# Performance work log

Hardware: AMD Instinct MI355X
Metric: run time of the kernel (lower is better)

The kernel has to match this reference:

```python
import jax, jax.numpy as jnp
import numpy as np

N = 50000
E = 800000
IN_C = 64
OUT_C = 64
K = 2
GATE_C = IN_C + OUT_C
LAMBDA_MAX = 2.0


def _lap_norm(edge_index, edge_weight, n):
    # PyG ChebConv norm: sym Laplacian L = I - D^-1/2 A D^-1/2, scaled 2L/lmax - I.
    # With lambda_max=2 the diagonal term is (2/lmax)*1 - 1 = 0, so only the
    # off-diagonal weights -(2/lmax) * w_norm remain.
    row, col = edge_index[0], edge_index[1]
    deg = jax.ops.segment_sum(edge_weight, row, num_segments=n)
    dinv = jnp.where(deg > 0, jax.lax.rsqrt(jnp.where(deg > 0, deg, 1.0)), 0.0)
    lw = -(2.0 / LAMBDA_MAX) * edge_weight * dinv[row] * dinv[col]
    diag = jnp.full((n,), 2.0 / LAMBDA_MAX - 1.0, edge_weight.dtype)  # zeros for lmax=2
    return row, col, lw, diag


def _cheb_conv(x, row, col, lw, diag, Ws, b):
    # Ws: [K, C_in, C_out]; Tx_0 = x, Tx_1 = L_hat x, Tx_k = 2 L_hat Tx_{k-1} - Tx_{k-2}
    n = x.shape[0]

    def prop(h):  # L_hat @ h  via edge gather/scatter + diagonal
        msg = lw[:, None] * h[col]                      # [E, C]
        return jax.ops.segment_sum(msg, row, num_segments=n) + diag[:, None] * h

    Tx0 = x
    out = Tx0 @ Ws[0]
    Tx1 = prop(x)
    out = out + Tx1 @ Ws[1]
    for k in range(2, K):
        Tx2 = 2.0 * prop(Tx1) - Tx0
        out = out + Tx2 @ Ws[k]
        Tx0, Tx1 = Tx1, Tx2
    return out + b


def setup_inputs() -> dict:
    key = jax.random.key(0)
    ks = jax.random.split(key, 10)
    scale = 1.0 / np.sqrt(GATE_C)
    x = jax.random.normal(ks[0], (N, IN_C), jnp.float32)
    edge_index = jax.random.randint(ks[1], (2, E), 0, N, jnp.int64)
    edge_weight = jax.random.uniform(ks[2], (E,), jnp.float32)
    hidden_state = jax.random.normal(ks[3], (N, OUT_C), jnp.float32)
    Wz = jax.random.normal(ks[4], (K, GATE_C, OUT_C), jnp.float32) * scale
    Wr = jax.random.normal(ks[5], (K, GATE_C, OUT_C), jnp.float32) * scale
    Wh = jax.random.normal(ks[6], (K, GATE_C, OUT_C), jnp.float32) * scale
    bz = jnp.zeros((OUT_C,), jnp.float32)
    br = jnp.zeros((OUT_C,), jnp.float32)
    bh = jnp.zeros((OUT_C,), jnp.float32)
    return {"x": x, "edge_index": edge_index, "edge_weight": edge_weight,
            "hidden_state": hidden_state, "Wz": Wz, "bz": bz,
            "Wr": Wr, "br": br, "Wh": Wh, "bh": bh}


def reference(x, edge_index, edge_weight, hidden_state, Wz, bz, Wr, br, Wh, bh):
    n = x.shape[0]
    row, col, lw, diag = _lap_norm(edge_index, edge_weight, n)
    gate_input = jnp.concatenate([x, hidden_state], axis=-1)          # [N, GATE_C]
    z = jax.nn.sigmoid(_cheb_conv(gate_input, row, col, lw, diag, Wz, bz))
    r = jax.nn.sigmoid(_cheb_conv(gate_input, row, col, lw, diag, Wr, br))
    cand_in = jnp.concatenate([x, r * hidden_state], axis=-1)
    h_tilde = jnp.tanh(_cheb_conv(cand_in, row, col, lw, diag, Wh, bh))
    return (1.0 - z) * hidden_state + z * h_tilde
```

## Files before the change

### kernel.cpp

```cpp
#include <hip/hip_runtime.h>
#include <cstdint>

#define N_NODES 50000
#define N_EDGES 800000
#define C 64
#define SLOTS 64
#define B_N 120
#define NB 417
#define PCAP 2560
#define STG_BLOCKS 126
#define STG_CHUNK 6350

typedef __attribute__((ext_vector_type(8))) short bf16x8;
typedef __attribute__((ext_vector_type(4))) float f32x4;

static constexpr size_t OFF_GCUR = 0;
static constexpr size_t OFF_DINV = 512;
static constexpr size_t OFF_CNT  = 50688;
static constexpr size_t OFF_BZR  = 100864;
static constexpr size_t OFF_BH   = 117248;
static constexpr size_t OFF_CSR  = 125440;
static constexpr size_t OFF_XH   = OFF_CSR + (size_t)N_NODES * 64;
static constexpr size_t OFF_XB   = OFF_XH + (size_t)N_NODES * C;
static constexpr size_t OFF_HB   = OFF_XB + (size_t)N_NODES * C / 2;
static constexpr size_t OFF_PXB  = OFF_HB + (size_t)N_NODES * C / 2;
static constexpr size_t OFF_PHB  = OFF_PXB + (size_t)N_NODES * C / 2;
static constexpr size_t OFF_RHB  = OFF_PHB + (size_t)N_NODES * C / 2;
static constexpr size_t OFF_RHD  = OFF_RHB + (size_t)N_NODES * C / 2;
static constexpr size_t OFF_STG  = OFF_PXB;

__device__ __forceinline__ short f2bf(float f) {
    unsigned u = __float_as_uint(f);
    u += 0x7fffu + ((u >> 16) & 1u);
    return (short)(u >> 16);
}
__device__ __forceinline__ float bf_lo(unsigned v) { return __uint_as_float(v << 16); }
__device__ __forceinline__ float bf_hi(unsigned v) { return __uint_as_float(v & 0xffff0000u); }
__device__ __forceinline__ float bfu(unsigned short v) { return __uint_as_float((unsigned)v << 16); }
__device__ __forceinline__ float fast_sigmoid(float v) { return 1.f / (1.f + __expf(-v)); }
__device__ __forceinline__ float fast_tanh(float v) { return 1.f - 2.f / (__expf(2.f * v) + 1.f); }

__global__ __launch_bounds__(256) void zero_pack_kernel(
        int* __restrict__ gcur,
        const float* __restrict__ Wz, const float* __restrict__ Wr,
        const float* __restrict__ Wh,
        short* __restrict__ Bzr, short* __restrict__ Bh) {
    if (blockIdx.x == 24) {
        gcur[threadIdx.x] = 0;
        gcur[256 + threadIdx.x] = 0;
        return;
    }
    int gid = blockIdx.x * 256 + threadIdx.x;
    if (gid < 4096) {
        int ktct = gid >> 6, lane = gid & 63;
        int kt = ktct >> 3, ct = ktct & 7;
        int colg = ct * 16 + (lane & 15);
        int k0 = kt * 32 + (lane >> 4) * 8;
        const float* W = (colg < 64) ? Wz : Wr;
        int c = colg & 63;
        short v[8];
        #pragma unroll
        for (int j = 0; j < 8; ++j) {
            int k = k0 + j;
            v[j] = f2bf(W[(k >> 7) * (128 * 64) + (k & 127) * 64 + c]);
        }
        *(bf16x8*)(Bzr + (size_t)ktct * 512 + lane * 8) = *(bf16x8*)v;
    } else {
        int idx = gid - 4096;
        int ktct = idx >> 6, lane = idx & 63;
        int kt = ktct >> 2, ct = ktct & 3;
        int colg = ct * 16 + (lane & 15);
        int k0 = kt * 32 + (lane >> 4) * 8;
        short v[8];
        #pragma unroll
        for (int j = 0; j < 8; ++j) {
            int k = k0 + j;
            v[j] = f2bf(Wh[(k >> 7) * (128 * 64) + (k & 127) * 64 + colg]);
        }
        *(bf16x8*)(Bh + (size_t)ktct * 512 + lane * 8) = *(bf16x8*)v;
    }
}

__global__ __launch_bounds__(512) void stage_kernel(
        const int* __restrict__ row, const int* __restrict__ col,
        const float* __restrict__ w,
        int* __restrict__ gcur, uint2* __restrict__ stg) {
    __shared__ int lcnt[NB];
    __shared__ int lbase[NB];
    int tid = threadIdx.x;
    int e0 = blockIdx.x * STG_CHUNK;
    int e1 = min(e0 + STG_CHUNK, N_EDGES);
    for (int i = tid; i < NB; i += 512) lcnt[i] = 0;
    __syncthreads();
    for (int e = e0 + tid; e < e1; e += 512)
        atomicAdd(&lcnt[row[e] / B_N], 1);
    __syncthreads();
    for (int i = tid; i < NB; i += 512) {
        int c = lcnt[i];
        lbase[i] = c ? atomicAdd(&gcur[i], c) : 0;
        lcnt[i] = 0;
    }
    __syncthreads();
    for (int e = e0 + tid; e < e1; e += 512) {
        int r = row[e];
        int b = r / B_N;
        int off = atomicAdd(&lcnt[b], 1);
        int pos = lbase[b] + off;
        unsigned cw = ((unsigned)col[e] << 16) | (unsigned short)f2bf(w[e]);
        if (pos < PCAP)
            stg[(size_t)b * PCAP + pos] = make_uint2((unsigned)(r - b * B_N), cw);
    }
}

__global__ __launch_bounds__(256) void sort_kernel(
        const int* __restrict__ gcur, const uint2* __restrict__ stg,
        const float* __restrict__ x, const float* __restrict__ h,
        unsigned* __restrict__ csr, int* __restrict__ cnt, float* __restrict__ dinv,
        unsigned* __restrict__ xh,
        unsigned short* __restrict__ xb, unsigned short* __restrict__ hb) {
    __shared__ int lcnt[B_N];
    __shared__ int lbase[B_N];
    __shared__ float ldeg[B_N];
    __shared__ float ldv[B_N];
    __shared__ int scanb[128];
    __shared__ unsigned lbuf[PCAP];
    __shared__ unsigned char lnode[PCAP];
    int b = blockIdx.x, tid = threadIdx.x;
    int n0 = b * B_N;
    int m = min(gcur[b], PCAP);
    for (int i = tid; i < B_N; i += 256) { lcnt[i] = 0; ldeg[i] = 0.f; }
    __syncthreads();
    const uint2* s = stg + (size_t)b * PCAP;
    for (int i = tid; i < m; i += 256) {
        uint2 e = s[i];
        atomicAdd(&lcnt[e.x], 1);
        atomicAdd(&ldeg[e.x], bf_lo(e.y));
    }
    __syncthreads();
    if (tid < 128) scanb[tid] = (tid < B_N) ? lcnt[tid] : 0;
    __syncthreads();
    for (int d = 1; d < 128; d <<= 1) {
        int v = 0;
        if (tid < 128 && tid >= d) v = scanb[tid - d];
        __syncthreads();
        if (tid < 128) scanb[tid] += v;
        __syncthreads();
    }
    if (tid < B_N) { lbase[tid] = scanb[tid] - lcnt[tid]; lcnt[tid] = 0; }
    __syncthreads();
    for (int i = tid; i < m; i += 256) {
        uint2 e = s[i];
        int off = atomicAdd(&lcnt[e.x], 1);
        int p = lbase[e.x] + off;
        lbuf[p] = e.y;
        lnode[p] = (unsigned char)e.x;
    }
    __syncthreads();
    for (int i = tid; i < m; i += 256) {
        int nl = lnode[i];
        int pos = i - lbase[nl];
        csr[(size_t)(n0 + nl) * SLOTS + pos] = lbuf[i];
    }
    for (int i = tid; i < B_N * 8; i += 256) {
        int nl = i >> 3;
        int node = n0 + nl;
        if (node >= N_NODES) continue;
        int mm = min(lcnt[nl], SLOTS);
        int pe = (mm + 7) & ~7;
        int idx = mm + (i & 7);
        if (idx < pe) csr[(size_t)node * SLOTS + idx] = 0u;
    }
    if (tid < B_N) {
        int node = n0 + tid;
        if (node < N_NODES) {
            cnt[node] = lcnt[tid];
            float d = ldeg[tid];
            float dv = (d > 0.f) ? rsqrtf(d) : 0.f;
            dinv[node] = dv;
            ldv[tid] = dv;
        } else ldv[tid] = 0.f;
    }
    __syncthreads();
    for (int i = tid; i < B_N * 16; i += 256) {
        int g = n0 * 16 + i;
        if (g >= N_NODES * 16) continue;
        float dv = ldv[i >> 4];
        float4 xv = ((const float4*)x)[g];
        float4 hv = ((const float4*)h)[g];
        uint4 o;
        o.x = ((unsigned)(unsigned short)f2bf(hv.x * dv) << 16) | (unsigned short)f2bf(xv.x * dv);
        o.y = ((unsigned)(unsigned short)f2bf(hv.y * dv) << 16) | (unsigned short)f2bf(xv.y * dv);
        o.z = ((unsigned)(unsigned short)f2bf(hv.z * dv) << 16) | (unsigned short)f2bf(xv.z * dv);
        o.w = ((unsigned)(unsigned short)f2bf(hv.w * dv) << 16) | (unsigned short)f2bf(xv.w * dv);
        ((uint4*)xh)[g] = o;
        ((short4*)xb)[g] = make_short4(f2bf(xv.x), f2bf(xv.y), f2bf(xv.z), f2bf(xv.w));
        ((short4*)hb)[g] = make_short4(f2bf(hv.x), f2bf(hv.y), f2bf(hv.z), f2bf(hv.w));
    }
}

__global__ __launch_bounds__(256) void prop_gemm_zr_kernel(
        const int* __restrict__ cnt, const unsigned* __restrict__ csr,
        const float* __restrict__ dinv, const unsigned* __restrict__ xh,
        const unsigned short* __restrict__ xb, const unsigned short* __restrict__ hb,
        const short* __restrict__ Bzr,
        const float* __restrict__ bz, const float* __restrict__ br,
        unsigned short* __restrict__ Pxb,
        float* __restrict__ z, unsigned short* __restrict__ rhb,
        unsigned short* __restrict__ rhd) {
    __shared__ __align__(16) unsigned short lpx[16][72];
    __shared__ __align__(16) unsigned short lph[16][72];
    int tid = threadIdx.x;
    int wid = tid >> 6, lane = tid & 63;
    int node0 = blockIdx.x * 16;

    #pragma unroll
    for (int i = 0; i < 2; ++i) {
        int nlA = wid * 4 + i * 2;
        int nA = node0 + nlA;
        int2 cc = *(const int2*)(cnt + nA);
        int gqA = (min(cc.x, SLOTS) + 7) >> 3;
        int gqB = (min(cc.y, SLOTS) + 7) >> 3;
        const uint4* sA = (const uint4*)(csr + (size_t)nA * SLOTS);
        const uint4* sB = (const uint4*)(csr + (size_t)(nA + 1) * SLOTS);
        float axA = 0.f, ahA = 0.f, axB = 0.f, ahB = 0.f;
        int gmax = max(gqA, gqB);
        for (int g = 0; g < gmax; ++g) {
            bool doA = g < gqA, doB = g < gqB;
            uint4 a0, a1, b0, b1;
            unsigned va0, va1, va2, va3, va4, va5, va6, va7;
            unsigned vb0, vb1, vb2, vb3, vb4, vb5, vb6, vb7;
            if (doA) { a0 = sA[2 * g]; a1 = sA[2 * g + 1]; }
            if (doB) { b0 = sB[2 * g]; b1 = sB[2 * g + 1]; }
            if (doA) {
                va0 = xh[(a0.x >> 16) * C + lane];
                va1 = xh[(a0.y >> 16) * C + lane];
                va2 = xh[(a0.z >> 16) * C + lane];
                va3 = xh[(a0.w >> 16) * C + lane];
                va4 = xh[(a1.x >> 16) * C + lane];
                va5 = xh[(a1.y >> 16) * C + lane];
                va6 = xh[(a1.z >> 16) * C + lane];
                va7 = xh[(a1.w >> 16) * C + lane];
            }
            if (doB) {
                vb0 = xh[(b0.x >> 16) * C + lane];
                vb1 = xh[(b0.y >> 16) * C + lane];
                vb2 = xh[(b0.z >> 16) * C + lane];
                vb3 = xh[(b0.w >> 16) * C + lane];
                vb4 = xh[(b1.x >> 16) * C + lane];
                vb5 = xh[(b1.y >> 16) * C + lane];
                vb6 = xh[(b1.z >> 16) * C + lane];
                vb7 = xh[(b1.w >> 16) * C + lane];
            }
            if (doA) {
                float w0 = bf_lo(a0.x), w1 = bf_lo(a0.y), w2 = bf_lo(a0.z), w3 = bf_lo(a0.w);
                float w4 = bf_lo(a1.x), w5 = bf_lo(a1.y), w6 = bf_lo(a1.z), w7 = bf_lo(a1.w);
                axA = fmaf(w0, bf_lo(va0), axA);  ahA = fmaf(w0, bf_hi(va0), ahA);
                axA = fmaf(w1, bf_lo(va1), axA);  ahA = fmaf(w1, bf_hi(va1), ahA);
                axA = fmaf(w2, bf_lo(va2), axA);  ahA = fmaf(w2, bf_hi(va2), ahA);
                axA = fmaf(w3, bf_lo(va3), axA);  ahA = fmaf(w3, bf_hi(va3), ahA);
                axA = fmaf(w4, bf_lo(va4), axA);  ahA = fmaf(w4, bf_hi(va4), ahA);
                axA = fmaf(w5, bf_lo(va5), axA);  ahA = fmaf(w5, bf_hi(va5), ahA);
                axA = fmaf(w6, bf_lo(va6), axA);  ahA = fmaf(w6, bf_hi(va6), ahA);
                axA = fmaf(w7, bf_lo(va7), axA);  ahA = fmaf(w7, bf_hi(va7), ahA);
            }
            if (doB) {
                float w0 = bf_lo(b0.x), w1 = bf_lo(b0.y), w2 = bf_lo(b0.z), w3 = bf_lo(b0.w);
                float w4 = bf_lo(b1.x), w5 = bf_lo(b1.y), w6 = bf_lo(b1.z), w7 = bf_lo(b1.w);
                axB = fmaf(w0, bf_lo(vb0), axB);  ahB = fmaf(w0, bf_hi(vb0), ahB);
                axB = fmaf(w1, bf_lo(vb1), axB);  ahB = fmaf(w1, bf_hi(vb1), ahB);
                axB = fmaf(w2, bf_lo(vb2), axB);  ahB = fmaf(w2, bf_hi(vb2), ahB);
                axB = fmaf(w3, bf_lo(vb3), axB);  ahB = fmaf(w3, bf_hi(vb3), ahB);
                axB = fmaf(w4, bf_lo(vb4), axB);  ahB = fmaf(w4, bf_hi(vb4), ahB);
                axB = fmaf(w5, bf_lo(vb5), axB);  ahB = fmaf(w5, bf_hi(vb5), ahB);
                axB = fmaf(w6, bf_lo(vb6), axB);  ahB = fmaf(w6, bf_hi(vb6), ahB);
                axB = fmaf(w7, bf_lo(vb7), axB);  ahB = fmaf(w7, bf_hi(vb7), ahB);
            }
        }
        float2 dv = *(const float2*)(dinv + nA);
        unsigned short pxA = (unsigned short)f2bf(-dv.x * axA);
        unsigned short phA = (unsigned short)f2bf(-dv.x * ahA);
        unsigned short pxB = (unsigned short)f2bf(-dv.y * axB);
        unsigned short phB = (unsigned short)f2bf(-dv.y * ahB);
        lpx[nlA][lane] = pxA;      lph[nlA][lane] = phA;
        lpx[nlA + 1][lane] = pxB;  lph[nlA + 1][lane] = phB;
        Pxb[(size_t)nA * C + lane] = pxA;
        Pxb[(size_t)(nA + 1) * C + lane] = pxB;
    }
    __syncthreads();

    int q = lane >> 4;
    int nl = lane & 15;
    f32x4 acc[2];
    acc[0] = (f32x4){0.f, 0.f, 0.f, 0.f};
    acc[1] = (f32x4){0.f, 0.f, 0.f, 0.f};
    const bf16x8* Bp = (const bf16x8*)Bzr;
    #pragma unroll
    for (int kt = 0; kt < 8; ++kt) {
        bf16x8 a;
        if (kt < 4) {
            const unsigned short* src = (kt < 2) ? xb : hb;
            a = *(const bf16x8*)(src + (size_t)(node0 + nl) * C + (kt & 1) * 32 + q * 8);
        } else {
            const unsigned short* src = (kt < 6) ? &lpx[0][0] : &lph[0][0];
            a = *(const bf16x8*)(src + nl * 72 + (kt & 1) * 32 + q * 8);
        }
        #pragma unroll
        for (int c2 = 0; c2 < 2; ++c2) {
            int ct = wid * 2 + c2;
            bf16x8 bfr = Bp[(kt * 8 + ct) * 64 + lane];
            acc[c2] = __builtin_amdgcn_mfma_f32_16x16x32_bf16(a, bfr, acc[c2], 0, 0, 0);
        }
    }

    if (wid < 2) {
        #pragma unroll
        for (int c2 = 0; c2 < 2; ++c2) {
            int colg = (wid * 2 + c2) * 16 + nl;
            float bias = bz[colg];
            #pragma unroll
            for (int r = 0; r < 4; ++r) {
                int node = node0 + q * 4 + r;
                z[(size_t)node * C + colg] = fast_sigmoid(acc[c2][r] + bias);
            }
        }
    } else {
        float dv[4];
        #pragma unroll
        for (int r = 0; r < 4; ++r) dv[r] = dinv[node0 + q * 4 + r];
        #pragma unroll
        for (int c2 = 0; c2 < 2; ++c2) {
            int oc = (wid * 2 + c2 - 4) * 16 + nl;
            float bias = br[oc];
            #pragma unroll
            for (int r = 0; r < 4; ++r) {
                int node = node0 + q * 4 + r;
                float sg = fast_sigmoid(acc[c2][r] + bias);
                float rhv = sg * bfu(hb[(size_t)node * C + oc]);
                rhb[(size_t)node * C + oc] = (unsigned short)f2bf(rhv);
                rhd[(size_t)node * C + oc] = (unsigned short)f2bf(rhv * dv[r]);
            }
        }
    }
}

__global__ __launch_bounds__(256) void prop_gemm_h_kernel(
        const int* __restrict__ cnt, const unsigned* __restrict__ csr,
        const float* __restrict__ dinv, const unsigned short* __restrict__ rhd,
        const unsigned short* __restrict__ xb, const unsigned short* __restrict__ rhb,
        const unsigned short* __restrict__ Pxb,
        const short* __restrict__ Bh, const float* __restrict__ bh,
        const float* __restrict__ z, const float* __restrict__ h,
        float* __restrict__ out) {
    __shared__ __align__(16) unsigned short lpr[16][72];
    int tid = threadIdx.x;
    int wid = tid >> 6, lane = tid & 63;
    int node0 = blockIdx.x * 16;

    #pragma unroll
    for (int i = 0; i < 2; ++i) {
        int nlA = wid * 4 + i * 2;
        int nA = node0 + nlA;
        int2 cc = *(const int2*)(cnt + nA);
        int gqA = (min(cc.x, SLOTS) + 7) >> 3;
        int gqB = (min(cc.y, SLOTS) + 7) >> 3;
        const uint4* sA = (const uint4*)(csr + (size_t)nA * SLOTS);
        const uint4* sB = (const uint4*)(csr + (size_t)(nA + 1) * SLOTS);
        float accA = 0.f, accB = 0.f;
        int gmax = max(gqA, gqB);
        for (int g = 0; g < gmax; ++g) {
            bool doA = g < gqA, doB = g < gqB;
            uint4 a0, a1, b0, b1;
            unsigned short va0, va1, va2, va3, va4, va5, va6, va7;
            unsigned short vb0, vb1, vb2, vb3, vb4, vb5, vb6, vb7;
            if (doA) { a0 = sA[2 * g]; a1 = sA[2 * g + 1]; }
            if (doB) { b0 = sB[2 * g]; b1 = sB[2 * g + 1]; }
            if (doA) {
                va0 = rhd[(a0.x >> 16) * C + lane];
                va1 = rhd[(a0.y >> 16) * C + lane];
                va2 = rhd[(a0.z >> 16) * C + lane];
                va3 = rhd[(a0.w >> 16) * C + lane];
                va4 = rhd[(a1.x >> 16) * C + lane];
                va5 = rhd[(a1.y >> 16) * C + lane];
                va6 = rhd[(a1.z >> 16) * C + lane];
                va7 = rhd[(a1.w >> 16) * C + lane];
            }
            if (doB) {
                vb0 = rhd[(b0.x >> 16) * C + lane];
                vb1 = rhd[(b0.y >> 16) * C + lane];
                vb2 = rhd[(b0.z >> 16) * C + lane];
                vb3 = rhd[(b0.w >> 16) * C + lane];
                vb4 = rhd[(b1.x >> 16) * C + lane];
                vb5 = rhd[(b1.y >> 16) * C + lane];
                vb6 = rhd[(b1.z >> 16) * C + lane];
                vb7 = rhd[(b1.w >> 16) * C + lane];
            }
            if (doA) {
                accA = fmaf(bf_lo(a0.x), bfu(va0), accA);
                accA = fmaf(bf_lo(a0.y), bfu(va1), accA);
                accA = fmaf(bf_lo(a0.z), bfu(va2), accA);
                accA = fmaf(bf_lo(a0.w), bfu(va3), accA);
                accA = fmaf(bf_lo(a1.x), bfu(va4), accA);
                accA = fmaf(bf_lo(a1.y), bfu(va5), accA);
                accA = fmaf(bf_lo(a1.z), bfu(va6), accA);
                accA = fmaf(bf_lo(a1.w), bfu(va7), accA);
            }
            if (doB) {
                accB = fmaf(bf_lo(b0.x), bfu(vb0), accB);
                accB = fmaf(bf_lo(b0.y), bfu(vb1), accB);
                accB = fmaf(bf_lo(b0.z), bfu(vb2), accB);
                accB = fmaf(bf_lo(b0.w), bfu(vb3), accB);
                accB = fmaf(bf_lo(b1.x), bfu(vb4), accB);
                accB = fmaf(bf_lo(b1.y), bfu(vb5), accB);
                accB = fmaf(bf_lo(b1.z), bfu(vb6), accB);
                accB = fmaf(bf_lo(b1.w), bfu(vb7), accB);
            }
        }
        float2 dv = *(const float2*)(dinv + nA);
        lpr[nlA][lane]     = (unsigned short)f2bf(-dv.x * accA);
        lpr[nlA + 1][lane] = (unsigned short)f2bf(-dv.y * accB);
    }
    __syncthreads();

    int q = lane >> 4;
    int nl = lane & 15;
    f32x4 acc = (f32x4){0.f, 0.f, 0.f, 0.f};
    const bf16x8* Bp = (const bf16x8*)Bh;
    #pragma unroll
    for (int kt = 0; kt < 8; ++kt) {
        bf16x8 a;
        if (kt < 6) {
            const unsigned short* src = (kt < 2) ? xb : (kt < 4) ? rhb : Pxb;
            a = *(const bf16x8*)(src + (size_t)(node0 + nl) * C + (kt & 1) * 32 + q * 8);
        } else {
            a = *(const bf16x8*)(&lpr[0][0] + nl * 72 + (kt & 1) * 32 + q * 8);
        }
        bf16x8 bfr = Bp[(kt * 4 + wid) * 64 + lane];
        acc = __builtin_amdgcn_mfma_f32_16x16x32_bf16(a, bfr, acc, 0, 0, 0);
    }

    int oc = wid * 16 + nl;
    float bias = bh[oc];
    #pragma unroll
    for (int r = 0; r < 4; ++r) {
        int node = node0 + q * 4 + r;
        float ht = fast_tanh(acc[r] + bias);
        float zz = z[(size_t)node * C + oc];
        float hv = h[(size_t)node * C + oc];
        out[(size_t)node * C + oc] = (1.f - zz) * hv + zz * ht;
    }
}

extern "C" void kernel_launch(void* const* d_in, const int* in_sizes, int n_in,
                              void* d_out, int out_size, void* d_ws, size_t ws_size,
                              hipStream_t stream) {
    const float* x    = (const float*)d_in[0];
    const int*   eidx = (const int*)  d_in[1];
    const float* w    = (const float*)d_in[2];
    const float* h    = (const float*)d_in[3];
    const float* Wz   = (const float*)d_in[4];
    const float* bz   = (const float*)d_in[5];
    const float* Wr   = (const float*)d_in[6];
    const float* br   = (const float*)d_in[7];
    const float* Wh   = (const float*)d_in[8];
    const float* bh   = (const float*)d_in[9];
    float* out = (float*)d_out;
    float* ws  = (float*)d_ws;

    const int* row = eidx;
    const int* col = eidx + N_EDGES;

    int*            gcur = (int*)(ws + OFF_GCUR);
    float*          dinv = ws + OFF_DINV;
    int*            cnt  = (int*)(ws + OFF_CNT);
    unsigned*       csr  = (unsigned*)(ws + OFF_CSR);
    short*          Bzr  = (short*)(ws + OFF_BZR);
    short*          Bh   = (short*)(ws + OFF_BH);
    unsigned*       xh   = (unsigned*)(ws + OFF_XH);
    unsigned short* xb   = (unsigned short*)(ws + OFF_XB);
    unsigned short* hb   = (unsigned short*)(ws + OFF_HB);
    unsigned short* Pxb  = (unsigned short*)(ws + OFF_PXB);
    unsigned short* rhb  = (unsigned short*)(ws + OFF_RHB);
    unsigned short* rhd  = (unsigned short*)(ws + OFF_RHD);
    uint2*          stg  = (uint2*)(ws + OFF_STG);
    float*          z    = out;

    zero_pack_kernel<<<25, 256, 0, stream>>>(gcur, Wz, Wr, Wh, Bzr, Bh);

    stage_kernel<<<STG_BLOCKS, 512, 0, stream>>>(row, col, w, gcur, stg);

    sort_kernel<<<NB, 256, 0, stream>>>(gcur, stg, x, h, csr, cnt, dinv, xh, xb, hb);

    prop_gemm_zr_kernel<<<N_NODES / 16, 256, 0, stream>>>(
        cnt, csr, dinv, xh, xb, hb, Bzr, bz, br, Pxb, z, rhb, rhd);

    prop_gemm_h_kernel<<<N_NODES / 16, 256, 0, stream>>>(
        cnt, csr, dinv, rhd, xb, rhb, Pxb, Bh, bh, z, h, out);
}
```

Baseline: 209.9 us.

## Software-pipeline CSR gather loops with double-buffered neighbor loads

```diff
diff --git a/kernel.cpp b/kernel.cpp
--- a/kernel.cpp
+++ b/kernel.cpp
@@ -13,6 +13,8 @@
 
 typedef __attribute__((ext_vector_type(8))) short bf16x8;
 typedef __attribute__((ext_vector_type(4))) float f32x4;
+typedef __attribute__((ext_vector_type(8))) unsigned u32x8;
+typedef __attribute__((ext_vector_type(8))) unsigned short u16x8;
 
 static constexpr size_t OFF_GCUR = 0;
 static constexpr size_t OFF_DINV = 512;
@@ -39,6 +41,41 @@
 __device__ __forceinline__ float bfu(unsigned short v) { return __uint_as_float((unsigned)v << 16); }
 __device__ __forceinline__ float fast_sigmoid(float v) { return 1.f / (1.f + __expf(-v)); }
 __device__ __forceinline__ float fast_tanh(float v) { return 1.f - 2.f / (__expf(2.f * v) + 1.f); }
+
+#define ISS8(buf, q0, q1, TBL) \
+    buf[0] = TBL[(q0.x >> 16) * C + lane]; \
+    buf[1] = TBL[(q0.y >> 16) * C + lane]; \
+    buf[2] = TBL[(q0.z >> 16) * C + lane]; \
+    buf[3] = TBL[(q0.w >> 16) * C + lane]; \
+    buf[4] = TBL[(q1.x >> 16) * C + lane]; \
+    buf[5] = TBL[(q1.y >> 16) * C + lane]; \
+    buf[6] = TBL[(q1.z >> 16) * C + lane]; \
+    buf[7] = TBL[(q1.w >> 16) * C + lane];
+
+#define WEXT(W, q0, q1) \
+    float W##0 = bf_lo(q0.x), W##1 = bf_lo(q0.y), W##2 = bf_lo(q0.z), \
+          W##3 = bf_lo(q0.w), W##4 = bf_lo(q1.x), W##5 = bf_lo(q1.y), \
+          W##6 = bf_lo(q1.z), W##7 = bf_lo(q1.w);
+
+#define FMA2x8(buf, W, ax, ah) \
+    ax = fmaf(W##0, bf_lo(buf[0]), ax); ah = fmaf(W##0, bf_hi(buf[0]), ah); \
+    ax = fmaf(W##1, bf_lo(buf[1]), ax); ah = fmaf(W##1, bf_hi(buf[1]), ah); \
+    ax = fmaf(W##2, bf_lo(buf[2]), ax); ah = fmaf(W##2, bf_hi(buf[2]), ah); \
+    ax = fmaf(W##3, bf_lo(buf[3]), ax); ah = fmaf(W##3, bf_hi(buf[3]), ah); \
+    ax = fmaf(W##4, bf_lo(buf[4]), ax); ah = fmaf(W##4, bf_hi(buf[4]), ah); \
+    ax = fmaf(W##5, bf_lo(buf[5]), ax); ah = fmaf(W##5, bf_hi(buf[5]), ah); \
+    ax = fmaf(W##6, bf_lo(buf[6]), ax); ah = fmaf(W##6, bf_hi(buf[6]), ah); \
+    ax = fmaf(W##7, bf_lo(buf[7]), ax); ah = fmaf(W##7, bf_hi(buf[7]), ah);
+
+#define FMA1x8(buf, W, acc) \
+    acc = fmaf(W##0, bfu(buf[0]), acc); \
+    acc = fmaf(W##1, bfu(buf[1]), acc); \
+    acc = fmaf(W##2, bfu(buf[2]), acc); \
+    acc = fmaf(W##3, bfu(buf[3]), acc); \
+    acc = fmaf(W##4, bfu(buf[4]), acc); \
+    acc = fmaf(W##5, bfu(buf[5]), acc); \
+    acc = fmaf(W##6, bfu(buf[6]), acc); \
+    acc = fmaf(W##7, bfu(buf[7]), acc);
 
 __global__ __launch_bounds__(256) void zero_pack_kernel(
         int* __restrict__ gcur,
@@ -167,6 +204,7 @@
         if (node >= N_NODES) continue;
         int mm = min(lcnt[nl], SLOTS);
         int pe = (mm + 7) & ~7;
+        if (pe == 0) pe = 8;
         int idx = mm + (i & 7);
         if (idx < pe) csr[(size_t)node * SLOTS + idx] = 0u;
     }
@@ -218,62 +256,43 @@
         int nlA = wid * 4 + i * 2;
         int nA = node0 + nlA;
         int2 cc = *(const int2*)(cnt + nA);
-        int gqA = (min(cc.x, SLOTS) + 7) >> 3;
-        int gqB = (min(cc.y, SLOTS) + 7) >> 3;
+        int gqA = (min(cc.x, SLOTS) + 7) >> 3;  if (gqA < 1) gqA = 1;
+        int gqB = (min(cc.y, SLOTS) + 7) >> 3;  if (gqB < 1) gqB = 1;
+        int gmax = max(gqA, gqB);
         const uint4* sA = (const uint4*)(csr + (size_t)nA * SLOTS);
         const uint4* sB = (const uint4*)(csr + (size_t)(nA + 1) * SLOTS);
+        uint4 cA0 = sA[0], cA1 = sA[1], cB0 = sB[0], cB1 = sB[1];
+        uint4 nA0 = sA[2], nA1 = sA[3], nB0 = sB[2], nB1 = sB[3];
+        u32x8 XA, XB, YA, YB;
+        ISS8(XA, cA0, cA1, xh)
+        ISS8(XB, cB0, cB1, xh)
         float axA = 0.f, ahA = 0.f, axB = 0.f, ahB = 0.f;
-        int gmax = max(gqA, gqB);
-        for (int g = 0; g < gmax; ++g) {
-            bool doA = g < gqA, doB = g < gqB;
-            uint4 a0, a1, b0, b1;
-            unsigned va0, va1, va2, va3, va4, va5, va6, va7;
-            unsigned vb0, vb1, vb2, vb3, vb4, vb5, vb6, vb7;
-            if (doA) { a0 = sA[2 * g]; a1 = sA[2 * g + 1]; }
-            if (doB) { b0 = sB[2 * g]; b1 = sB[2 * g + 1]; }
-            if (doA) {
-                va0 = xh[(a0.x >> 16) * C + lane];
-                va1 = xh[(a0.y >> 16) * C + lane];
-                va2 = xh[(a0.z >> 16) * C + lane];
-                va3 = xh[(a0.w >> 16) * C + lane];
-                va4 = xh[(a1.x >> 16) * C + lane];
-                va5 = xh[(a1.y >> 16) * C + lane];
-                va6 = xh[(a1.z >> 16) * C + lane];
-                va7 = xh[(a1.w >> 16) * C + lane];
+        for (int g = 0; ; ) {
+            {
+                WEXT(wA, cA0, cA1)
+                WEXT(wB, cB0, cB1)
+                if (g + 1 < gqA) { ISS8(YA, nA0, nA1, xh) }
+                if (g + 1 < gqB) { ISS8(YB, nB0, nB1, xh) }
+                if (g + 2 < gmax) {
+                    cA0 = sA[2 * g + 4]; cA1 = sA[2 * g + 5];
+                    cB0 = sB[2 * g + 4]; cB1 = sB[2 * g + 5];
+                }
+                if (g < gqA) { FMA2x8(XA, wA, axA, ahA) }
+                if (g < gqB) { FMA2x8(XB, wB, axB, ahB) }
+                if (++g >= gmax) break;
             }
-            if (doB) {
-                vb0 = xh[(b0.x >> 16) * C + lane];
-                vb1 = xh[(b0.y >> 16) * C + lane];
-                vb2 = xh[(b0.z >> 16) * C + lane];
-                vb3 = xh[(b0.w >> 16) * C + lane];
-                vb4 = xh[(b1.x >> 16) * C + lane];
-                vb5 = xh[(b1.y >> 16) * C + lane];
-                vb6 = xh[(b1.z >> 16) * C + lane];
-                vb7 = xh[(b1.w >> 16) * C + lane];
-            }
-            if (doA) {
-                float w0 = bf_lo(a0.x), w1 = bf_lo(a0.y), w2 = bf_lo(a0.z), w3 = bf_lo(a0.w);
-                float w4 = bf_lo(a1.x), w5 = bf_lo(a1.y), w6 = bf_lo(a1.z), w7 = bf_lo(a1.w);
-                axA = fmaf(w0, bf_lo(va0), axA);  ahA = fmaf(w0, bf_hi(va0), ahA);
-                axA = fmaf(w1, bf_lo(va1), axA);  ahA = fmaf(w1, bf_hi(va1), ahA);
-                axA = fmaf(w2, bf_lo(va2), axA);  ahA = fmaf(w2, bf_hi(va2), ahA);
-                axA = fmaf(w3, bf_lo(va3), axA);  ahA = fmaf(w3, bf_hi(va3), ahA);
-                axA = fmaf(w4, bf_lo(va4), axA);  ahA = fmaf(w4, bf_hi(va4), ahA);
-                axA = fmaf(w5, bf_lo(va5), axA);  ahA = fmaf(w5, bf_hi(va5), ahA);
-                axA = fmaf(w6, bf_lo(va6), axA);  ahA = fmaf(w6, bf_hi(va6), ahA);
-                axA = fmaf(w7, bf_lo(va7), axA);  ahA = fmaf(w7, bf_hi(va7), ahA);
-            }
-            if (doB) {
-                float w0 = bf_lo(b0.x), w1 = bf_lo(b0.y), w2 = bf_lo(b0.z), w3 = bf_lo(b0.w);
-                float w4 = bf_lo(b1.x), w5 = bf_lo(b1.y), w6 = bf_lo(b1.z), w7 = bf_lo(b1.w);
-                axB = fmaf(w0, bf_lo(vb0), axB);  ahB = fmaf(w0, bf_hi(vb0), ahB);
-                axB = fmaf(w1, bf_lo(vb1), axB);  ahB = fmaf(w1, bf_hi(vb1), ahB);
-                axB = fmaf(w2, bf_lo(vb2), axB);  ahB = fmaf(w2, bf_hi(vb2), ahB);
-                axB = fmaf(w3, bf_lo(vb3), axB);  ahB = fmaf(w3, bf_hi(vb3), ahB);
-                axB = fmaf(w4, bf_lo(vb4), axB);  ahB = fmaf(w4, bf_hi(vb4), ahB);
-                axB = fmaf(w5, bf_lo(vb5), axB);  ahB = fmaf(w5, bf_hi(vb5), ahB);
-                axB = fmaf(w6, bf_lo(vb6), axB);  ahB = fmaf(w6, bf_hi(vb6), ahB);
-                axB = fmaf(w7, bf_lo(vb7), axB);  ahB = fmaf(w7, bf_hi(vb7), ahB);
+            {
+                WEXT(wA, nA0, nA1)
+                WEXT(wB, nB0, nB1)
+                if (g + 1 < gqA) { ISS8(XA, cA0, cA1, xh) }
+                if (g + 1 < gqB) { ISS8(XB, cB0, cB1, xh) }
+                if (g + 2 < gmax) {
+                    nA0 = sA[2 * g + 4]; nA1 = sA[2 * g + 5];
+                    nB0 = sB[2 * g + 4]; nB1 = sB[2 * g + 5];
+                }
+                if (g < gqA) { FMA2x8(YA, wA, axA, ahA) }
+                if (g < gqB) { FMA2x8(YB, wB, axB, ahB) }
+                if (++g >= gmax) break;
             }
         }
         float2 dv = *(const float2*)(dinv + nA);
@@ -361,58 +380,43 @@
         int nlA = wid * 4 + i * 2;
         int nA = node0 + nlA;
         int2 cc = *(const int2*)(cnt + nA);
-        int gqA = (min(cc.x, SLOTS) + 7) >> 3;
-        int gqB = (min(cc.y, SLOTS) + 7) >> 3;
+        int gqA = (min(cc.x, SLOTS) + 7) >> 3;  if (gqA < 1) gqA = 1;
+        int gqB = (min(cc.y, SLOTS) + 7) >> 3;  if (gqB < 1) gqB = 1;
+        int gmax = max(gqA, gqB);
         const uint4* sA = (const uint4*)(csr + (size_t)nA * SLOTS);
         const uint4* sB = (const uint4*)(csr + (size_t)(nA + 1) * SLOTS);
+        uint4 cA0 = sA[0], cA1 = sA[1], cB0 = sB[0], cB1 = sB[1];
+        uint4 nA0 = sA[2], nA1 = sA[3], nB0 = sB[2], nB1 = sB[3];
+        u16x8 XA, XB, YA, YB;
+        ISS8(XA, cA0, cA1, rhd)
+        ISS8(XB, cB0, cB1, rhd)
         float accA = 0.f, accB = 0.f;
-        int gmax = max(gqA, gqB);
-        for (int g = 0; g < gmax; ++g) {
-            bool doA = g < gqA, doB = g < gqB;
-            uint4 a0, a1, b0, b1;
-            unsigned short va0, va1, va2, va3, va4, va5, va6, va7;
-            unsigned short vb0, vb1, vb2, vb3, vb4, vb5, vb6, vb7;
-            if (doA) { a0 = sA[2 * g]; a1 = sA[2 * g + 1]; }
-            if (doB) { b0 = sB[2 * g]; b1 = sB[2 * g + 1]; }
-            if (doA) {
-                va0 = rhd[(a0.x >> 16) * C + lane];
-                va1 = rhd[(a0.y >> 16) * C + lane];
-                va2 = rhd[(a0.z >> 16) * C + lane];
-                va3 = rhd[(a0.w >> 16) * C + lane];
-                va4 = rhd[(a1.x >> 16) * C + lane];
-                va5 = rhd[(a1.y >> 16) * C + lane];
-                va6 = rhd[(a1.z >> 16) * C + lane];
-                va7 = rhd[(a1.w >> 16) * C + lane];
+        for (int g = 0; ; ) {
+            {
+                WEXT(wA, cA0, cA1)
+                WEXT(wB, cB0, cB1)
+                if (g + 1 < gqA) { ISS8(YA, nA0, nA1, rhd) }
+                if (g + 1 < gqB) { ISS8(YB, nB0, nB1, rhd) }
+                if (g + 2 < gmax) {
+                    cA0 = sA[2 * g + 4]; cA1 = sA[2 * g + 5];
+                    cB0 = sB[2 * g + 4]; cB1 = sB[2 * g + 5];
+                }
+                if (g < gqA) { FMA1x8(XA, wA, accA) }
+                if (g < gqB) { FMA1x8(XB, wB, accB) }
+                if (++g >= gmax) break;
             }
-            if (doB) {
-                vb0 = rhd[(b0.x >> 16) * C + lane];
-                vb1 = rhd[(b0.y >> 16) * C + lane];
-                vb2 = rhd[(b0.z >> 16) * C + lane];
-                vb3 = rhd[(b0.w >> 16) * C + lane];
-                vb4 = rhd[(b1.x >> 16) * C + lane];
-                vb5 = rhd[(b1.y >> 16) * C + lane];
-                vb6 = rhd[(b1.z >> 16) * C + lane];
-                vb7 = rhd[(b1.w >> 16) * C + lane];
-            }
-            if (doA) {
-                accA = fmaf(bf_lo(a0.x), bfu(va0), accA);
-                accA = fmaf(bf_lo(a0.y), bfu(va1), accA);
-                accA = fmaf(bf_lo(a0.z), bfu(va2), accA);
-                accA = fmaf(bf_lo(a0.w), bfu(va3), accA);
-                accA = fmaf(bf_lo(a1.x), bfu(va4), accA);
-                accA = fmaf(bf_lo(a1.y), bfu(va5), accA);
-                accA = fmaf(bf_lo(a1.z), bfu(va6), accA);
-                accA = fmaf(bf_lo(a1.w), bfu(va7), accA);
-            }
-            if (doB) {
-                accB = fmaf(bf_lo(b0.x), bfu(vb0), accB);
-                accB = fmaf(bf_lo(b0.y), bfu(vb1), accB);
-                accB = fmaf(bf_lo(b0.z), bfu(vb2), accB);
-                accB = fmaf(bf_lo(b0.w), bfu(vb3), accB);
-                accB = fmaf(bf_lo(b1.x), bfu(vb4), accB);
-                accB = fmaf(bf_lo(b1.y), bfu(vb5), accB);
-                accB = fmaf(bf_lo(b1.z), bfu(vb6), accB);
-                accB = fmaf(bf_lo(b1.w), bfu(vb7), accB);
+            {
+                WEXT(wA, nA0, nA1)
+                WEXT(wB, nB0, nB1)
+                if (g + 1 < gqA) { ISS8(XA, cA0, cA1, rhd) }
+                if (g + 1 < gqB) { ISS8(XB, cB0, cB1, rhd) }
+                if (g + 2 < gmax) {
+                    nA0 = sA[2 * g + 4]; nA1 = sA[2 * g + 5];
+                    nB0 = sB[2 * g + 4]; nB1 = sB[2 * g + 5];
+                }
+                if (g < gqA) { FMA1x8(YA, wA, accA) }
+                if (g < gqB) { FMA1x8(YB, wB, accB) }
+                if (++g >= gmax) break;
             }
         }
         float2 dv = *(const float2*)(dinv + nA);
```

New measurement: 217.7 us. 3.8% more time.

## Vectorize neighbor gathers with 4-edge lane groups and shuffle reduction

Applied to the files above, without the earlier changes.

```diff
diff --git a/kernel.cpp b/kernel.cpp
--- a/kernel.cpp
+++ b/kernel.cpp
@@ -39,6 +39,12 @@
 __device__ __forceinline__ float bfu(unsigned short v) { return __uint_as_float((unsigned)v << 16); }
 __device__ __forceinline__ float fast_sigmoid(float v) { return 1.f / (1.f + __expf(-v)); }
 __device__ __forceinline__ float fast_tanh(float v) { return 1.f - 2.f / (__expf(2.f * v) + 1.f); }
+__device__ __forceinline__ unsigned sel4u(unsigned a, unsigned b, unsigned c,
+                                          unsigned d, int g) {
+    unsigned r = (g & 1) ? b : a;
+    unsigned s = (g & 1) ? d : c;
+    return (g & 2) ? s : r;
+}
 
 __global__ __launch_bounds__(256) void zero_pack_kernel(
         int* __restrict__ gcur,
@@ -167,6 +173,7 @@
         if (node >= N_NODES) continue;
         int mm = min(lcnt[nl], SLOTS);
         int pe = (mm + 7) & ~7;
+        if (pe == 0) pe = 8;
         int idx = mm + (i & 7);
         if (idx < pe) csr[(size_t)node * SLOTS + idx] = 0u;
     }
@@ -210,7 +217,10 @@
     __shared__ __align__(16) unsigned short lpx[16][72];
     __shared__ __align__(16) unsigned short lph[16][72];
     int tid = threadIdx.x;
-    int wid = tid >> 6, lane = tid & 63;
+    int wid = __builtin_amdgcn_readfirstlane(tid >> 6);
+    int lane = tid & 63;
+    int lane15 = lane & 15;
+    int g4 = lane >> 4;
     int node0 = blockIdx.x * 16;
 
     #pragma unroll
@@ -222,69 +232,76 @@
         int gqB = (min(cc.y, SLOTS) + 7) >> 3;
         const uint4* sA = (const uint4*)(csr + (size_t)nA * SLOTS);
         const uint4* sB = (const uint4*)(csr + (size_t)(nA + 1) * SLOTS);
-        float axA = 0.f, ahA = 0.f, axB = 0.f, ahB = 0.f;
+        f32x4 axA = {0.f,0.f,0.f,0.f}, ahA = {0.f,0.f,0.f,0.f};
+        f32x4 axB = {0.f,0.f,0.f,0.f}, ahB = {0.f,0.f,0.f,0.f};
         int gmax = max(gqA, gqB);
         for (int g = 0; g < gmax; ++g) {
             bool doA = g < gqA, doB = g < gqB;
             uint4 a0, a1, b0, b1;
-            unsigned va0, va1, va2, va3, va4, va5, va6, va7;
-            unsigned vb0, vb1, vb2, vb3, vb4, vb5, vb6, vb7;
+            uint4 vA0, vA1, vB0, vB1;
+            unsigned eA0, eA1, eB0, eB1;
             if (doA) { a0 = sA[2 * g]; a1 = sA[2 * g + 1]; }
             if (doB) { b0 = sB[2 * g]; b1 = sB[2 * g + 1]; }
             if (doA) {
-                va0 = xh[(a0.x >> 16) * C + lane];
-                va1 = xh[(a0.y >> 16) * C + lane];
-                va2 = xh[(a0.z >> 16) * C + lane];
-                va3 = xh[(a0.w >> 16) * C + lane];
-                va4 = xh[(a1.x >> 16) * C + lane];
-                va5 = xh[(a1.y >> 16) * C + lane];
-                va6 = xh[(a1.z >> 16) * C + lane];
-                va7 = xh[(a1.w >> 16) * C + lane];
+                eA0 = sel4u(a0.x, a0.y, a0.z, a0.w, g4);
+                eA1 = sel4u(a1.x, a1.y, a1.z, a1.w, g4);
+                vA0 = *(const uint4*)(xh + (size_t)(eA0 >> 16) * C + lane15 * 4);
+                vA1 = *(const uint4*)(xh + (size_t)(eA1 >> 16) * C + lane15 * 4);
             }
             if (doB) {
-                vb0 = xh[(b0.x >> 16) * C + lane];
-                vb1 = xh[(b0.y >> 16) * C + lane];
-                vb2 = xh[(b0.z >> 16) * C + lane];
-                vb3 = xh[(b0.w >> 16) * C + lane];
-                vb4 = xh[(b1.x >> 16) * C + lane];
-                vb5 = xh[(b1.y >> 16) * C + lane];
-                vb6 = xh[(b1.z >> 16) * C + lane];
-                vb7 = xh[(b1.w >> 16) * C + lane];
+                eB0 = sel4u(b0.x, b0.y, b0.z, b0.w, g4);
+                eB1 = sel4u(b1.x, b1.y, b1.z, b1.w, g4);
+                vB0 = *(const uint4*)(xh + (size_t)(eB0 >> 16) * C + lane15 * 4);
+                vB1 = *(const uint4*)(xh + (size_t)(eB1 >> 16) * C + lane15 * 4);
             }
             if (doA) {
-                float w0 = bf_lo(a0.x), w1 = bf_lo(a0.y), w2 = bf_lo(a0.z), w3 = bf_lo(a0.w);
-                float w4 = bf_lo(a1.x), w5 = bf_lo(a1.y), w6 = bf_lo(a1.z), w7 = bf_lo(a1.w);
-                axA = fmaf(w0, bf_lo(va0), axA);  ahA = fmaf(w0, bf_hi(va0), ahA);
-                axA = fmaf(w1, bf_lo(va1), axA);  ahA = fmaf(w1, bf_hi(va1), ahA);
-                axA = fmaf(w2, bf_lo(va2), axA);  ahA = fmaf(w2, bf_hi(va2), ahA);
-                axA = fmaf(w3, bf_lo(va3), axA);  ahA = fmaf(w3, bf_hi(va3), ahA);
-                axA = fmaf(w4, bf_lo(va4), axA);  ahA = fmaf(w4, bf_hi(va4), ahA);
-                axA = fmaf(w5, bf_lo(va5), axA);  ahA = fmaf(w5, bf_hi(va5), ahA);
-                axA = fmaf(w6, bf_lo(va6), axA);  ahA = fmaf(w6, bf_hi(va6), ahA);
-                axA = fmaf(w7, bf_lo(va7), axA);  ahA = fmaf(w7, bf_hi(va7), ahA);
+                float w0 = bf_lo(eA0), w1 = bf_lo(eA1);
+                axA[0] = fmaf(w0, bf_lo(vA0.x), axA[0]); ahA[0] = fmaf(w0, bf_hi(vA0.x), ahA[0]);
+                axA[1] = fmaf(w0, bf_lo(vA0.y), axA[1]); ahA[1] = fmaf(w0, bf_hi(vA0.y), ahA[1]);
+                axA[2] = fmaf(w0, bf_lo(vA0.z), axA[2]); ahA[2] = fmaf(w0, bf_hi(vA0.z), ahA[2]);
+                axA[3] = fmaf(w0, bf_lo(vA0.w), axA[3]); ahA[3] = fmaf(w0, bf_hi(vA0.w), ahA[3]);
+                axA[0] = fmaf(w1, bf_lo(vA1.x), axA[0]); ahA[0] = fmaf(w1, bf_hi(vA1.x), ahA[0]);
+                axA[1] = fmaf(w1, bf_lo(vA1.y), axA[1]); ahA[1] = fmaf(w1, bf_hi(vA1.y), ahA[1]);
+                axA[2] = fmaf(w1, bf_lo(vA1.z), axA[2]); ahA[2] = fmaf(w1, bf_hi(vA1.z), ahA[2]);
+                axA[3] = fmaf(w1, bf_lo(vA1.w), axA[3]); ahA[3] = fmaf(w1, bf_hi(vA1.w), ahA[3]);
             }
             if (doB) {
-                float w0 = bf_lo(b0.x), w1 = bf_lo(b0.y), w2 = bf_lo(b0.z), w3 = bf_lo(b0.w);
-                float w4 = bf_lo(b1.x), w5 = bf_lo(b1.y), w6 = bf_lo(b1.z), w7 = bf_lo(b1.w);
-                axB = fmaf(w0, bf_lo(vb0), axB);  ahB = fmaf(w0, bf_hi(vb0), ahB);
-                axB = fmaf(w1, bf_lo(vb1), axB);  ahB = fmaf(w1, bf_hi(vb1), ahB);
-                axB = fmaf(w2, bf_lo(vb2), axB);  ahB = fmaf(w2, bf_hi(vb2), ahB);
-                axB = fmaf(w3, bf_lo(vb3), axB);  ahB = fmaf(w3, bf_hi(vb3), ahB);
-                axB = fmaf(w4, bf_lo(vb4), axB);  ahB = fmaf(w4, bf_hi(vb4), ahB);
-                axB = fmaf(w5, bf_lo(vb5), axB);  ahB = fmaf(w5, bf_hi(vb5), ahB);
-                axB = fmaf(w6, bf_lo(vb6), axB);  ahB = fmaf(w6, bf_hi(vb6), ahB);
-                axB = fmaf(w7, bf_lo(vb7), axB);  ahB = fmaf(w7, bf_hi(vb7), ahB);
-            }
-        }
-        float2 dv = *(const float2*)(dinv + nA);
-        unsigned short pxA = (unsigned short)f2bf(-dv.x * axA);
-        unsigned short phA = (unsigned short)f2bf(-dv.x * ahA);
-        unsigned short pxB = (unsigned short)f2bf(-dv.y * axB);
-        unsigned short phB = (unsigned short)f2bf(-dv.y * ahB);
-        lpx[nlA][lane] = pxA;      lph[nlA][lane] = phA;
-        lpx[nlA + 1][lane] = pxB;  lph[nlA + 1][lane] = phB;
-        Pxb[(size_t)nA * C + lane] = pxA;
-        Pxb[(size_t)(nA + 1) * C + lane] = pxB;
+                float w0 = bf_lo(eB0), w1 = bf_lo(eB1);
+                axB[0] = fmaf(w0, bf_lo(vB0.x), axB[0]); ahB[0] = fmaf(w0, bf_hi(vB0.x), ahB[0]);
+                axB[1] = fmaf(w0, bf_lo(vB0.y), axB[1]); ahB[1] = fmaf(w0, bf_hi(vB0.y), ahB[1]);
+                axB[2] = fmaf(w0, bf_lo(vB0.z), axB[2]); ahB[2] = fmaf(w0, bf_hi(vB0.z), ahB[2]);
+                axB[3] = fmaf(w0, bf_lo(vB0.w), axB[3]); ahB[3] = fmaf(w0, bf_hi(vB0.w), ahB[3]);
+                axB[0] = fmaf(w1, bf_lo(vB1.x), axB[0]); ahB[0] = fmaf(w1, bf_hi(vB1.x), ahB[0]);
+                axB[1] = fmaf(w1, bf_lo(vB1.y), axB[1]); ahB[1] = fmaf(w1, bf_hi(vB1.y), ahB[1]);
+                axB[2] = fmaf(w1, bf_lo(vB1.z), axB[2]); ahB[2] = fmaf(w1, bf_hi(vB1.z), ahB[2]);
+                axB[3] = fmaf(w1, bf_lo(vB1.w), axB[3]); ahB[3] = fmaf(w1, bf_hi(vB1.w), ahB[3]);
+            }
+        }
+        #pragma unroll
+        for (int j = 0; j < 4; ++j) {
+            axA[j] += __shfl_xor(axA[j], 16, 64); axA[j] += __shfl_xor(axA[j], 32, 64);
+            ahA[j] += __shfl_xor(ahA[j], 16, 64); ahA[j] += __shfl_xor(ahA[j], 32, 64);
+            axB[j] += __shfl_xor(axB[j], 16, 64); axB[j] += __shfl_xor(axB[j], 32, 64);
+            ahB[j] += __shfl_xor(ahB[j], 16, 64); ahB[j] += __shfl_xor(ahB[j], 32, 64);
+        }
+        float2 dvp = *(const float2*)(dinv + nA);
+        if (g4 == 0) {
+            float sA1 = -dvp.x, sB1 = -dvp.y;
+            short4 pxA = make_short4(f2bf(sA1 * axA[0]), f2bf(sA1 * axA[1]),
+                                     f2bf(sA1 * axA[2]), f2bf(sA1 * axA[3]));
+            short4 phA = make_short4(f2bf(sA1 * ahA[0]), f2bf(sA1 * ahA[1]),
+                                     f2bf(sA1 * ahA[2]), f2bf(sA1 * ahA[3]));
+            short4 pxB = make_short4(f2bf(sB1 * axB[0]), f2bf(sB1 * axB[1]),
+                                     f2bf(sB1 * axB[2]), f2bf(sB1 * axB[3]));
+            short4 phB = make_short4(f2bf(sB1 * ahB[0]), f2bf(sB1 * ahB[1]),
+                                     f2bf(sB1 * ahB[2]), f2bf(sB1 * ahB[3]));
+            *(short4*)(&lpx[nlA][lane15 * 4]) = pxA;
+            *(short4*)(&lph[nlA][lane15 * 4]) = phA;
+            *(short4*)(&lpx[nlA + 1][lane15 * 4]) = pxB;
+            *(short4*)(&lph[nlA + 1][lane15 * 4]) = phB;
+            *(short4*)(Pxb + (size_t)nA * C + lane15 * 4) = pxA;
+            *(short4*)(Pxb + (size_t)(nA + 1) * C + lane15 * 4) = pxB;
+        }
     }
     __syncthreads();
 
@@ -353,7 +370,10 @@
         float* __restrict__ out) {
     __shared__ __align__(16) unsigned short lpr[16][72];
     int tid = threadIdx.x;
-    int wid = tid >> 6, lane = tid & 63;
+    int wid = __builtin_amdgcn_readfirstlane(tid >> 6);
+    int lane = tid & 63;
+    int lane15 = lane & 15;
+    int g4 = lane >> 4;
     int node0 = blockIdx.x * 16;
 
     #pragma unroll
@@ -365,59 +385,65 @@
         int gqB = (min(cc.y, SLOTS) + 7) >> 3;
         const uint4* sA = (const uint4*)(csr + (size_t)nA * SLOTS);
         const uint4* sB = (const uint4*)(csr + (size_t)(nA + 1) * SLOTS);
-        float accA = 0.f, accB = 0.f;
+        f32x4 aA = {0.f,0.f,0.f,0.f}, aB = {0.f,0.f,0.f,0.f};
         int gmax = max(gqA, gqB);
         for (int g = 0; g < gmax; ++g) {
             bool doA = g < gqA, doB = g < gqB;
             uint4 a0, a1, b0, b1;
-            unsigned short va0, va1, va2, va3, va4, va5, va6, va7;
-            unsigned short vb0, vb1, vb2, vb3, vb4, vb5, vb6, vb7;
+            uint2 vA0, vA1, vB0, vB1;
+            unsigned eA0, eA1, eB0, eB1;
             if (doA) { a0 = sA[2 * g]; a1 = sA[2 * g + 1]; }
             if (doB) { b0 = sB[2 * g]; b1 = sB[2 * g + 1]; }
             if (doA) {
-                va0 = rhd[(a0.x >> 16) * C + lane];
-                va1 = rhd[(a0.y >> 16) * C + lane];
-                va2 = rhd[(a0.z >> 16) * C + lane];
-                va3 = rhd[(a0.w >> 16) * C + lane];
-                va4 = rhd[(a1.x >> 16) * C + lane];
-                va5 = rhd[(a1.y >> 16) * C + lane];
-                va6 = rhd[(a1.z >> 16) * C + lane];
-                va7 = rhd[(a1.w >> 16) * C + lane];
+                eA0 = sel4u(a0.x, a0.y, a0.z, a0.w, g4);
+                eA1 = sel4u(a1.x, a1.y, a1.z, a1.w, g4);
+                vA0 = *(const uint2*)(rhd + (size_t)(eA0 >> 16) * C + lane15 * 4);
+                vA1 = *(const uint2*)(rhd + (size_t)(eA1 >> 16) * C + lane15 * 4);
             }
             if (doB) {
-                vb0 = rhd[(b0.x >> 16) * C + lane];
-                vb1 = rhd[(b0.y >> 16) * C + lane];
-                vb2 = rhd[(b0.z >> 16) * C + lane];
-                vb3 = rhd[(b0.w >> 16) * C + lane];
-                vb4 = rhd[(b1.x >> 16) * C + lane];
-                vb5 = rhd[(b1.y >> 16) * C + lane];
-                vb6 = rhd[(b1.z >> 16) * C + lane];
-                vb7 = rhd[(b1.w >> 16) * C + lane];
+                eB0 = sel4u(b0.x, b0.y, b0.z, b0.w, g4);
+                eB1 = sel4u(b1.x, b1.y, b1.z, b1.w, g4);
+                vB0 = *(const uint2*)(rhd + (size_t)(eB0 >> 16) * C + lane15 * 4);
+                vB1 = *(const uint2*)(rhd + (size_t)(eB1 >> 16) * C + lane15 * 4);
             }
             if (doA) {
-                accA = fmaf(bf_lo(a0.x), bfu(va0), accA);
-                accA = fmaf(bf_lo(a0.y), bfu(va1), accA);
-                accA = fmaf(bf_lo(a0.z), bfu(va2), accA);
-                accA = fmaf(bf_lo(a0.w), bfu(va3), accA);
-                accA = fmaf(bf_lo(a1.x), bfu(va4), accA);
-                accA = fmaf(bf_lo(a1.y), bfu(va5), accA);
-                accA = fmaf(bf_lo(a1.z), bfu(va6), accA);
-                accA = fmaf(bf_lo(a1.w), bfu(va7), accA);
+                float w0 = bf_lo(eA0), w1 = bf_lo(eA1);
+                aA[0] = fmaf(w0, bf_lo(vA0.x), aA[0]);
+                aA[1] = fmaf(w0, bf_hi(vA0.x), aA[1]);
+                aA[2] = fmaf(w0, bf_lo(vA0.y), aA[2]);
+                aA[3] = fmaf(w0, bf_hi(vA0.y), aA[3]);
+                aA[0] = fmaf(w1, bf_lo(vA1.x), aA[0]);
+                aA[1] = fmaf(w1, bf_hi(vA1.x), aA[1]);
+                aA[2] = fmaf(w1, bf_lo(vA1.y), aA[2]);
+                aA[3] = fmaf(w1, bf_hi(vA1.y), aA[3]);
             }
             if (doB) {
-                accB = fmaf(bf_lo(b0.x), bfu(vb0), accB);
-                accB = fmaf(bf_lo(b0.y), bfu(vb1), accB);
-                accB = fmaf(bf_lo(b0.z), bfu(vb2), accB);
-                accB = fmaf(bf_lo(b0.w), bfu(vb3), accB);
-                accB = fmaf(bf_lo(b1.x), bfu(vb4), accB);
-                accB = fmaf(bf_lo(b1.y), bfu(vb5), accB);
-                accB = fmaf(bf_lo(b1.z), bfu(vb6), accB);
-                accB = fmaf(bf_lo(b1.w), bfu(vb7), accB);
-            }
-        }
-        float2 dv = *(const float2*)(dinv + nA);
-        lpr[nlA][lane]     = (unsigned short)f2bf(-dv.x * accA);
-        lpr[nlA + 1][lane] = (unsigned short)f2bf(-dv.y * accB);
+                float w0 = bf_lo(eB0), w1 = bf_lo(eB1);
+                aB[0] = fmaf(w0, bf_lo(vB0.x), aB[0]);
+                aB[1] = fmaf(w0, bf_hi(vB0.x), aB[1]);
+                aB[2] = fmaf(w0, bf_lo(vB0.y), aB[2]);
+                aB[3] = fmaf(w0, bf_hi(vB0.y), aB[3]);
+                aB[0] = fmaf(w1, bf_lo(vB1.x), aB[0]);
+                aB[1] = fmaf(w1, bf_hi(vB1.x), aB[1]);
+                aB[2] = fmaf(w1, bf_lo(vB1.y), aB[2]);
+                aB[3] = fmaf(w1, bf_hi(vB1.y), aB[3]);
+            }
+        }
+        #pragma unroll
+        for (int j = 0; j < 4; ++j) {
+            aA[j] += __shfl_xor(aA[j], 16, 64); aA[j] += __shfl_xor(aA[j], 32, 64);
+            aB[j] += __shfl_xor(aB[j], 16, 64); aB[j] += __shfl_xor(aB[j], 32, 64);
+        }
+        float2 dvp = *(const float2*)(dinv + nA);
+        if (g4 == 0) {
+            float sA1 = -dvp.x, sB1 = -dvp.y;
+            short4 prA = make_short4(f2bf(sA1 * aA[0]), f2bf(sA1 * aA[1]),
+                                     f2bf(sA1 * aA[2]), f2bf(sA1 * aA[3]));
+            short4 prB = make_short4(f2bf(sB1 * aB[0]), f2bf(sB1 * aB[1]),
+                                     f2bf(sB1 * aB[2]), f2bf(sB1 * aB[3]));
+            *(short4*)(&lpr[nlA][lane15 * 4]) = prA;
+            *(short4*)(&lpr[nlA + 1][lane15 * 4]) = prB;
+        }
     }
     __syncthreads();
 
```

Measured after the change: 209.1 us. No clear change (-0.4%).
